# Kernel optimization log

Measured on AMD Instinct MI355X. Metric: run time of the kernel, lower is better.

The kernel has to match this reference:

```python
import jax, jax.numpy as jnp
import numpy as np

B, C, H, W = 4, 64, 64, 64
C8 = C // 8


def cl_attention(x, gamma):
    # DANet CAM-style channel attention: [B,C,H,W] -> [B,C,H,W]
    b, c, h, w = x.shape
    xf = x.reshape(b, c, h * w)                       # b c n
    energy = jnp.einsum('bcn,bdn->bcd', xf, xf)       # b c c
    energy = jnp.max(energy, axis=-1, keepdims=True) - energy
    attn = jax.nn.softmax(energy, axis=-1)
    out = jnp.einsum('bcd,bdn->bcn', attn, xf).reshape(b, c, h, w)
    return gamma * out + x


def setup_inputs() -> dict:
    key = jax.random.key(0)
    ks = jax.random.split(key, 8)
    s = 0.02
    return {
        'cnn_feat': jax.random.normal(ks[0], (B, C, H, W), jnp.float32),
        'vit_feat': jax.random.normal(ks[1], (B, C, H, W), jnp.float32),
        'Wq': jax.random.normal(ks[2], (C8, C), jnp.float32) * s,   # 1x1 conv kernel
        'bq': jnp.zeros((C8,), jnp.float32),
        'Wk': jax.random.normal(ks[3], (C8, C), jnp.float32) * s,
        'bk': jnp.zeros((C8,), jnp.float32),
        'Wv': jax.random.normal(ks[4], (C, C), jnp.float32) * s,
        'bv': jnp.zeros((C,), jnp.float32),
        'gamma': jnp.zeros((1,), jnp.float32),
        'gamma_cla_cnn': jnp.zeros((1,), jnp.float32),
        'gamma_cla_vit': jnp.zeros((1,), jnp.float32),
    }


def reference(cnn_feat, vit_feat, Wq, bq, Wk, bk, Wv, bv, gamma,
              gamma_cla_cnn, gamma_cla_vit):
    b, c, h, w = cnn_feat.shape
    n = h * w

    cnn_att = cl_attention(cnn_feat, gamma_cla_cnn)   # b c h w
    vit_att = cl_attention(vit_feat, gamma_cla_vit)   # b c h w

    # query: 1x1 conv -> view(b, C8, n) -> permute -> (b, n, C8)
    q = jnp.einsum('bchw,oc->bhwo', cnn_att, Wq).reshape(b, n, -1) + bq

    # vit: rearrange 'b c h w -> b (h w) c'
    vit_flat = vit_att.reshape(b, c, n).transpose(0, 2, 1)          # b n c
    k = vit_flat @ Wk.T + bk                                        # b n C8
    v = vit_flat @ Wv.T + bv                                        # b n C

    energy = jnp.einsum('bqd,bkd->bqk', q, k)                       # b n n
    attn = jax.nn.softmax(energy, axis=-1)
    out = jnp.einsum('bqk,bkc->bqc', attn, v)                       # b n c
    out = out.transpose(0, 2, 1).reshape(b, c, h, w)                # 'b (h w) c -> b c h w'
    return gamma * out + cnn_feat
```

## Files before the change

kernel.cpp:

```cpp
#include <hip/hip_runtime.h>
#include <hip/hip_bf16.h>

#define BSZ 4
#define CC 64
#define NN 4096
#define CN (CC*NN)
#define BCN (BSZ*CN)

typedef __attribute__((ext_vector_type(4))) float    f4v;
typedef __attribute__((ext_vector_type(4))) int      i4v;
typedef __attribute__((ext_vector_type(2))) int      i2v;
typedef __attribute__((ext_vector_type(2))) unsigned u2v;
typedef __attribute__((ext_vector_type(8))) short    s8v;

#define DPP_F(x_, ctrl_) __builtin_bit_cast(float, \
    __builtin_amdgcn_update_dpp(0, __builtin_bit_cast(int, (float)(x_)), (ctrl_), 0xf, 0xf, true))
#define QP_X1 0xB1

__device__ __forceinline__ unsigned pack_bf16(float lo, float hi) {
    unsigned l = __builtin_bit_cast(unsigned, lo);
    unsigned h = __builtin_bit_cast(unsigned, hi);
    return (h & 0xFFFF0000u) | (l >> 16);
}
__device__ __forceinline__ unsigned pack2(float lo, float hi) {
    float2 f2; f2.x = lo; f2.y = hi;
    __hip_bfloat162 h = __float22bfloat162_rn(f2);
    unsigned u;
    __builtin_memcpy(&u, &h, 4);
    return u;
}
__device__ __forceinline__ float blo(int d) {
    return __builtin_bit_cast(float, (unsigned)d << 16);
}
__device__ __forceinline__ float bhi(int d) {
    return __builtin_bit_cast(float, (unsigned)d & 0xFFFF0000u);
}

__global__ __launch_bounds__(256) void gram_k(const float* __restrict__ cnn,
                                              const float* __restrict__ vit,
                                              float* __restrict__ part) {
    __shared__ __align__(16) float sXT[128*68];
    int t = threadIdx.x;
    int blk = blockIdx.x;
    int ch = blk & 31, b = (blk >> 5) & 3, i2 = blk >> 7;
    const float* X = (i2 ? vit : cnn) + b * CN;
    int n0 = ch * 128;
#pragma unroll
    for (int j = 0; j < 8; j++) {
        int idx = t + j * 256;
        int c = idx >> 5, n4 = idx & 31;
        f4v val = *(const f4v*)&X[c * NN + n0 + n4 * 4];
        int base = (n4 * 4) * 68 + c;
        sXT[base]       = val[0];
        sXT[base + 68]  = val[1];
        sXT[base + 136] = val[2];
        sXT[base + 204] = val[3];
    }
    __syncthreads();
    int tc = (t & 15) * 4, td = (t >> 4) * 4;
    f4v acc[4];
#pragma unroll
    for (int i = 0; i < 4; i++) acc[i] = (f4v){0.f, 0.f, 0.f, 0.f};
    for (int k = 0; k < 128; k++) {
        f4v a  = *(const f4v*)&sXT[k * 68 + tc];
        f4v bb = *(const f4v*)&sXT[k * 68 + td];
#pragma unroll
        for (int i = 0; i < 4; i++) acc[i] += a[i] * bb;
    }
    float* dst = part + ch * 32768 + (i2 * 4 + b) * 4096;
#pragma unroll
    for (int i = 0; i < 4; i++) *(f4v*)&dst[(tc + i) * 64 + td] = acc[i];
}

__global__ void gred_k(const float* __restrict__ part, float* __restrict__ G) {
    int row = blockIdx.x;
    int d = threadIdx.x;
    float s = 0.f;
#pragma unroll 8
    for (int ch = 0; ch < 32; ch++) s += part[ch * 32768 + row * 64 + d];
    float mn = s;
#pragma unroll
    for (int off = 1; off < 64; off <<= 1) mn = fminf(mn, __shfl_xor(mn, off));
    float e = __expf(mn - s);
    float sm = e;
#pragma unroll
    for (int off = 1; off < 64; off <<= 1) sm += __shfl_xor(sm, off);
    G[row * 64 + d] = e / sm;
}

__global__ __launch_bounds__(256) void weff_k(const float* __restrict__ G,
                                              const float* __restrict__ Wq,
                                              const float* __restrict__ Wk,
                                              const float* __restrict__ Wv,
                                              const float* __restrict__ gcnn,
                                              const float* __restrict__ gvit,
                                              ushort* __restrict__ WeffB) {
    __shared__ float sA[8192];
    __shared__ float sWt[1024];
    int t = threadIdx.x;
    int b = blockIdx.x / 5, tile = blockIdx.x % 5;
    for (int i = t; i < 4096; i += 256) {
        sA[i]        = G[b * 4096 + i];
        sA[4096 + i] = G[(4 + b) * 4096 + i];
    }
    __syncthreads();
    float gc = *gcnn, gv = *gvit;
#pragma unroll
    for (int k = 0; k < 4; k++) {
        int idx = k * 256 + t;
        int r = idx >> 6, c = idx & 63;
        const float* Wrow; const float* A; float g;
        if (tile == 0) {
            if (r < 8) { Wrow = Wq + r * 64;       A = sA;        g = gc; }
            else       { Wrow = Wk + (r - 8) * 64; A = sA + 4096; g = gv; }
        } else         { Wrow = Wv + ((tile - 1) * 16 + r) * 64; A = sA + 4096; g = gv; }
        float s = 0.f;
#pragma unroll 8
        for (int d = 0; d < 64; d++) s += Wrow[d] * A[d * 64 + c];
        sWt[idx] = g * s + Wrow[c];
    }
    __syncthreads();
    if (t < 128) {
        int frag = t >> 6, lane = t & 63, m = lane & 15, q4 = lane >> 4;
        i4v o;
#pragma unroll
        for (int p = 0; p < 4; p++) {
            int c0 = frag * 32 + q4 * 8 + 2 * p;
            o[p] = (int)pack_bf16(sWt[m * 64 + c0], sWt[m * 64 + c0 + 1]);
        }
        *(i4v*)&WeffB[(size_t)(b * 10 + tile * 2 + frag) * 512 + lane * 8] = o;
    }
}

__global__ __launch_bounds__(256) void qkv_k(const float* __restrict__ cnn,
                                             const float* __restrict__ vit,
                                             const ushort* __restrict__ WeffB,
                                             const float* __restrict__ bq,
                                             const float* __restrict__ bk,
                                             const float* __restrict__ bv,
                                             ushort* __restrict__ qb, ushort* __restrict__ kb,
                                             ushort* __restrict__ vT) {
    int t = threadIdx.x;
    int b = blockIdx.x >> 6, n0 = (blockIdx.x & 63) * 64;
    int w = t >> 6, lane = t & 63, c15 = lane & 15, q4 = lane >> 4;
    int n = n0 + w * 16 + c15;
    const float LOG2E = 1.44269504f;

    s8v A[10];
    const ushort* WB = WeffB + (size_t)b * 5120 + lane * 8;
#pragma unroll
    for (int i = 0; i < 10; i++)
        A[i] = __builtin_bit_cast(s8v, *(const i4v*)(WB + (size_t)i * 512));

    s8v Bc[2], Bv[2];
#pragma unroll
    for (int f = 0; f < 2; f++) {
        i4v pc, pv;
#pragma unroll
        for (int p = 0; p < 4; p++) {
            int c0 = f * 32 + q4 * 8 + p * 2;
            size_t a0 = (size_t)b * CN + (size_t)c0 * NN + n;
            pc[p] = (int)pack_bf16(cnn[a0], cnn[a0 + NN]);
            pv[p] = (int)pack_bf16(vit[a0], vit[a0 + NN]);
        }
        Bc[f] = __builtin_bit_cast(s8v, pc);
        Bv[f] = __builtin_bit_cast(s8v, pv);
    }

    f4v acc = *(const f4v*)(bq + (q4 & 1) * 4);
    acc = __builtin_amdgcn_mfma_f32_16x16x32_bf16(A[0], Bc[0], acc, 0, 0, 0);
    acc = __builtin_amdgcn_mfma_f32_16x16x32_bf16(A[1], Bc[1], acc, 0, 0, 0);
    if (q4 < 2) {
        unsigned d0 = pack_bf16(acc[0] * LOG2E, acc[1] * LOG2E);
        unsigned d1 = pack_bf16(acc[2] * LOG2E, acc[3] * LOG2E);
        unsigned long long v = ((unsigned long long)d1 << 32) | d0;
        *(unsigned long long*)&qb[(size_t)(b * NN + n) * 8 + q4 * 4] = v;
    }
    acc = *(const f4v*)(bk + (q4 & 1) * 4);
    acc = __builtin_amdgcn_mfma_f32_16x16x32_bf16(A[0], Bv[0], acc, 0, 0, 0);
    acc = __builtin_amdgcn_mfma_f32_16x16x32_bf16(A[1], Bv[1], acc, 0, 0, 0);
    if (q4 >= 2) {
        unsigned d0 = pack_bf16(acc[0], acc[1]), d1 = pack_bf16(acc[2], acc[3]);
        unsigned long long v = ((unsigned long long)d1 << 32) | d0;
        *(unsigned long long*)&kb[(size_t)(b * NN + n) * 8 + (q4 - 2) * 4] = v;
    }
#pragma unroll
    for (int tile = 1; tile < 5; tile++) {
        acc = *(const f4v*)(bv + (tile - 1) * 16 + q4 * 4);
        acc = __builtin_amdgcn_mfma_f32_16x16x32_bf16(A[tile * 2],     Bv[0], acc, 0, 0, 0);
        acc = __builtin_amdgcn_mfma_f32_16x16x32_bf16(A[tile * 2 + 1], Bv[1], acc, 0, 0, 0);
#pragma unroll
        for (int r = 0; r < 4; r++) {
            float other = DPP_F(acc[r], QP_X1);
            unsigned pkd = (lane & 1) ? pack_bf16(other, acc[r])
                                      : pack_bf16(acc[r], other);
            if (!(lane & 1)) {
                int row = (tile - 1) * 16 + q4 * 4 + r;
                *(unsigned*)&vT[(size_t)(b * 64 + row) * NN + n] = pkd;
            }
        }
    }
}

__global__ __launch_bounds__(256, 2) void flash_k(const ushort* __restrict__ qb,
                                                  const ushort* __restrict__ kb,
                                                  const ushort* __restrict__ vT,
                                                  ushort* __restrict__ pOT,
                                                  float* __restrict__ pl) {
    __shared__ __align__(16) ushort Vlds[2 * 64 * 72];
    int t = threadIdx.x;
    int lane = t & 63, w = t >> 6;
    int c15 = lane & 15, q4 = lane >> 4;
    int blk = blockIdx.x;
    int s = blk >> 6, b = (blk >> 4) & 3, q0 = (blk & 15) * 256;

    s8v qB[4];
#pragma unroll
    for (int g = 0; g < 4; g++) {
        i4v qa = (i4v){0, 0, 0, 0};
        if (q4 == 0)
            qa = *(const i4v*)(qb + (size_t)(b * NN + q0 + w * 64 + g * 16 + c15) * 8);
        qB[g] = __builtin_bit_cast(s8v, qa);
    }

    f4v accO[4][4];
#pragma unroll
    for (int g = 0; g < 4; g++)
#pragma unroll
        for (int nt = 0; nt < 4; nt++) accO[g][nt] = (f4v){0.f, 0.f, 0.f, 0.f};
    float lacc[4] = {0.f, 0.f, 0.f, 0.f};

    const ushort* kbb = kb + (size_t)b * NN * 8 + (size_t)c15 * 8;

    int r = t >> 2, chk = t & 3;
    const ushort* vsrc = vT + (size_t)(b * 64 + r) * NN + chk * 16;
    int vdstoff = r * 72 + 32 * (chk >> 1) + 4 * (chk & 1);
    int vreadoff = c15 * 72 + 8 * q4;

    int kbase = s * 512;
    i4v bk_cur[4];
#pragma unroll
    for (int nt = 0; nt < 4; nt++)
        bk_cur[nt] = *(const i4v*)(kbb + (size_t)(kbase + nt * 16) * 8);
    i4v v0 = *(const i4v*)(vsrc + kbase);
    i4v v1 = *(const i4v*)(vsrc + kbase + 8);

    for (int kt = 0; kt < 8; kt++) {
        int k0 = kbase + kt * 64;
        ushort* vd = Vlds + (kt & 1) * 4608 + vdstoff;
        *(i2v*)(vd + 0)  = (i2v){v0[0], v0[1]};
        *(i2v*)(vd + 8)  = (i2v){v0[2], v0[3]};
        *(i2v*)(vd + 16) = (i2v){v1[0], v1[1]};
        *(i2v*)(vd + 24) = (i2v){v1[2], v1[3]};
        __syncthreads();

        const ushort* vb = Vlds + (kt & 1) * 4608 + vreadoff;
        i4v vA[2][4];
#pragma unroll
        for (int F = 0; F < 2; F++)
#pragma unroll
            for (int nt = 0; nt < 4; nt++)
                vA[F][nt] = *(const i4v*)(vb + nt * 16 * 72 + 32 * F);

        i4v bk_nxt[4];
        if (kt < 7) {
            v0 = *(const i4v*)(vsrc + k0 + 64);
            v1 = *(const i4v*)(vsrc + k0 + 64 + 8);
#pragma unroll
            for (int nt = 0; nt < 4; nt++)
                bk_nxt[nt] = *(const i4v*)(kbb + (size_t)(k0 + 64 + nt * 16) * 8);
        }

#pragma unroll
        for (int gp = 0; gp < 2; gp++) {
            f4v z = (f4v){0.f, 0.f, 0.f, 0.f};
            f4v S[2][4];
#pragma unroll
            for (int gg = 0; gg < 2; gg++)
#pragma unroll
                for (int nt = 0; nt < 4; nt++)
                    S[gg][nt] = __builtin_amdgcn_mfma_f32_16x16x32_bf16(
                        __builtin_bit_cast(s8v, bk_cur[nt]), qB[gp * 2 + gg],
                        z, 0, 0, 0);

            s8v Bp[2][2];
#pragma unroll
            for (int gg = 0; gg < 2; gg++) {
                f4v p[4];
                float ps = 0.f;
#pragma unroll
                for (int nt = 0; nt < 4; nt++)
#pragma unroll
                    for (int rr = 0; rr < 4; rr++) {
                        p[nt][rr] = __builtin_amdgcn_exp2f(S[gg][nt][rr]);
                        ps += p[nt][rr];
                    }
#pragma unroll
                for (int F = 0; F < 2; F++) {
                    i4v bp;
                    bp[0] = (int)pack2(p[2 * F][0],     p[2 * F][1]);
                    bp[1] = (int)pack2(p[2 * F][2],     p[2 * F][3]);
                    bp[2] = (int)pack2(p[2 * F + 1][0], p[2 * F + 1][1]);
                    bp[3] = (int)pack2(p[2 * F + 1][2], p[2 * F + 1][3]);
                    Bp[gg][F] = __builtin_bit_cast(s8v, bp);
                }
                lacc[gp * 2 + gg] += ps;
            }

#pragma unroll
            for (int F = 0; F < 2; F++)
#pragma unroll
                for (int gg = 0; gg < 2; gg++)
#pragma unroll
                    for (int nt = 0; nt < 4; nt++)
                        accO[gp * 2 + gg][nt] =
                            __builtin_amdgcn_mfma_f32_16x16x32_bf16(
                                __builtin_bit_cast(s8v, vA[F][nt]), Bp[gg][F],
                                accO[gp * 2 + gg][nt], 0, 0, 0);
        }
        if (kt < 7) {
#pragma unroll
            for (int nt = 0; nt < 4; nt++) bk_cur[nt] = bk_nxt[nt];
        }
    }

#pragma unroll
    for (int g = 0; g < 4; g++) {
        lacc[g] += __shfl_xor(lacc[g], 16);
        lacc[g] += __shfl_xor(lacc[g], 32);
    }

#pragma unroll
    for (int g = 0; g < 4; g++) {
        int qg = q0 + w * 64 + g * 16 + c15;
#pragma unroll
        for (int nt = 0; nt < 4; nt++) {
            int cg = nt * 4 + q4;
            u2v d;
            d[0] = pack2(accO[g][nt][0], accO[g][nt][1]);
            d[1] = pack2(accO[g][nt][2], accO[g][nt][3]);
            *(u2v*)&pOT[((size_t)((s * 4 + b) * 16 + cg) * NN + qg) * 4] = d;
        }
        if (q4 == 0)
            pl[(size_t)(s * 4 + b) * NN + qg] = lacc[g];
    }
}

__global__ __launch_bounds__(256) void comb_k(const ushort* __restrict__ pOT,
                                              const float* __restrict__ pl,
                                              const float* __restrict__ cnn,
                                              const float* __restrict__ gamma,
                                              float* __restrict__ out) {
    int t = threadIdx.x;
    int b = blockIdx.x >> 6, n0 = (blockIdx.x & 63) * 64;
    int nq = t & 15, cl = t >> 4;
    int n = n0 + nq * 4;
    f4v L = (f4v){0.f, 0.f, 0.f, 0.f};
#pragma unroll
    for (int s = 0; s < 8; s++)
        L += *(const f4v*)&pl[(size_t)(s * 4 + b) * NN + n];
    float g = *gamma;
    f4v rv;
#pragma unroll
    for (int j = 0; j < 4; j++) rv[j] = g / L[j];

    f4v Oc[4];
#pragma unroll
    for (int cc = 0; cc < 4; cc++) Oc[cc] = (f4v){0.f, 0.f, 0.f, 0.f};
#pragma unroll
    for (int s = 0; s < 8; s++) {
        const ushort* src = pOT + ((size_t)((s * 4 + b) * 16 + cl) * NN + n) * 4;
        i4v a  = *(const i4v*)src;
        i4v bb = *(const i4v*)(src + 8);
        Oc[0][0] += blo(a[0]);  Oc[1][0] += bhi(a[0]);
        Oc[2][0] += blo(a[1]);  Oc[3][0] += bhi(a[1]);
        Oc[0][1] += blo(a[2]);  Oc[1][1] += bhi(a[2]);
        Oc[2][1] += blo(a[3]);  Oc[3][1] += bhi(a[3]);
        Oc[0][2] += blo(bb[0]); Oc[1][2] += bhi(bb[0]);
        Oc[2][2] += blo(bb[1]); Oc[3][2] += bhi(bb[1]);
        Oc[0][3] += blo(bb[2]); Oc[1][3] += bhi(bb[2]);
        Oc[2][3] += blo(bb[3]); Oc[3][3] += bhi(bb[3]);
    }
#pragma unroll
    for (int cc = 0; cc < 4; cc++) {
        size_t gi = (size_t)(b * 64 + cl * 4 + cc) * NN + n;
        f4v cv = *(const f4v*)&cnn[gi];
        *(f4v*)&out[gi] = Oc[cc] * rv + cv;
    }
}

extern "C" void kernel_launch(void* const* d_in, const int* in_sizes, int n_in,
                              void* d_out, int out_size, void* d_ws, size_t ws_size,
                              hipStream_t stream) {
    const float* cnn  = (const float*)d_in[0];
    const float* vit  = (const float*)d_in[1];
    const float* Wq   = (const float*)d_in[2];
    const float* bq   = (const float*)d_in[3];
    const float* Wk   = (const float*)d_in[4];
    const float* bk   = (const float*)d_in[5];
    const float* Wv   = (const float*)d_in[6];
    const float* bv   = (const float*)d_in[7];
    const float* gam  = (const float*)d_in[8];
    const float* gcnn = (const float*)d_in[9];
    const float* gvit = (const float*)d_in[10];
    float* out = (float*)d_out;

    float* ws = (float*)d_ws;
    ushort* pOT   = (ushort*)ws;
    float*  part  = ws;
    float*  G     = ws + 8388608;
    ushort* WeffB = (ushort*)(ws + 8421376);
    ushort* qb    = (ushort*)(ws + 8431616);
    ushort* kb    = (ushort*)(ws + 8497152);
    ushort* vT    = (ushort*)(ws + 8562688);
    float*  pl    = ws + 9086976;

    gram_k <<<256, 256, 0, stream>>>(cnn, vit, part);
    gred_k <<<512, 64,  0, stream>>>(part, G);
    weff_k <<<20,  256, 0, stream>>>(G, Wq, Wk, Wv, gcnn, gvit, WeffB);
    qkv_k  <<<256, 256, 0, stream>>>(cnn, vit, WeffB, bq, bk, bv, qb, kb, vT);
    flash_k<<<512, 256, 0, stream>>>(qb, kb, vT, pOT, pl);
    comb_k <<<256, 256, 0, stream>>>(pOT, pl, cnn, gam, out);
}
```

Before: 129.7 us.

## Rebalance flash split-K: fewer key splits, smaller query tiles, prioritize MFMA

The flash kernel now uses 128 queries per block (32 per wave) and 4 key splits of 1024 keys each, instead of 256 queries per block and 8 splits of 512. This halves the partial outputs that comb_k must read and reduce, and lowers per-wave register pressure. It also adds s_setprio around the PV MFMA block and unroll pragmas on the flash and gram loops. In exchange, each loaded K/V tile is reused by fewer queries, so global and LDS traffic per useful FLOP goes up. The grid size is unchanged at 512 blocks.

```diff
diff --git a/kernel.cpp b/kernel.cpp
--- a/kernel.cpp
+++ b/kernel.cpp
@@ -61,6 +61,7 @@
     f4v acc[4];
 #pragma unroll
     for (int i = 0; i < 4; i++) acc[i] = (f4v){0.f, 0.f, 0.f, 0.f};
+#pragma unroll 4
     for (int k = 0; k < 128; k++) {
         f4v a  = *(const f4v*)&sXT[k * 68 + tc];
         f4v bb = *(const f4v*)&sXT[k * 68 + td];
@@ -212,23 +213,23 @@
     int lane = t & 63, w = t >> 6;
     int c15 = lane & 15, q4 = lane >> 4;
     int blk = blockIdx.x;
-    int s = blk >> 6, b = (blk >> 4) & 3, q0 = (blk & 15) * 256;
-
-    s8v qB[4];
-#pragma unroll
-    for (int g = 0; g < 4; g++) {
+    int s = blk >> 7, b = (blk >> 5) & 3, q0 = (blk & 31) * 128;
+
+    s8v qB[2];
+#pragma unroll
+    for (int g = 0; g < 2; g++) {
         i4v qa = (i4v){0, 0, 0, 0};
         if (q4 == 0)
-            qa = *(const i4v*)(qb + (size_t)(b * NN + q0 + w * 64 + g * 16 + c15) * 8);
+            qa = *(const i4v*)(qb + (size_t)(b * NN + q0 + w * 32 + g * 16 + c15) * 8);
         qB[g] = __builtin_bit_cast(s8v, qa);
     }
 
-    f4v accO[4][4];
-#pragma unroll
-    for (int g = 0; g < 4; g++)
+    f4v accO[2][4];
+#pragma unroll
+    for (int g = 0; g < 2; g++)
 #pragma unroll
         for (int nt = 0; nt < 4; nt++) accO[g][nt] = (f4v){0.f, 0.f, 0.f, 0.f};
-    float lacc[4] = {0.f, 0.f, 0.f, 0.f};
+    float lacc[2] = {0.f, 0.f};
 
     const ushort* kbb = kb + (size_t)b * NN * 8 + (size_t)c15 * 8;
 
@@ -237,7 +238,7 @@
     int vdstoff = r * 72 + 32 * (chk >> 1) + 4 * (chk & 1);
     int vreadoff = c15 * 72 + 8 * q4;
 
-    int kbase = s * 512;
+    int kbase = s * 1024;
     i4v bk_cur[4];
 #pragma unroll
     for (int nt = 0; nt < 4; nt++)
@@ -245,7 +246,8 @@
     i4v v0 = *(const i4v*)(vsrc + kbase);
     i4v v1 = *(const i4v*)(vsrc + kbase + 8);
 
-    for (int kt = 0; kt < 8; kt++) {
+#pragma unroll 2
+    for (int kt = 0; kt < 16; kt++) {
         int k0 = kbase + kt * 64;
         ushort* vd = Vlds + (kt & 1) * 4608 + vdstoff;
         *(i2v*)(vd + 0)  = (i2v){v0[0], v0[1]};
@@ -263,7 +265,7 @@
                 vA[F][nt] = *(const i4v*)(vb + nt * 16 * 72 + 32 * F);
 
         i4v bk_nxt[4];
-        if (kt < 7) {
+        if (kt < 15) {
             v0 = *(const i4v*)(vsrc + k0 + 64);
             v1 = *(const i4v*)(vsrc + k0 + 64 + 8);
 #pragma unroll
@@ -271,68 +273,67 @@
                 bk_nxt[nt] = *(const i4v*)(kbb + (size_t)(k0 + 64 + nt * 16) * 8);
         }
 
-#pragma unroll
-        for (int gp = 0; gp < 2; gp++) {
-            f4v z = (f4v){0.f, 0.f, 0.f, 0.f};
-            f4v S[2][4];
-#pragma unroll
-            for (int gg = 0; gg < 2; gg++)
+        f4v z = (f4v){0.f, 0.f, 0.f, 0.f};
+        f4v S[2][4];
+#pragma unroll
+        for (int g = 0; g < 2; g++)
+#pragma unroll
+            for (int nt = 0; nt < 4; nt++)
+                S[g][nt] = __builtin_amdgcn_mfma_f32_16x16x32_bf16(
+                    __builtin_bit_cast(s8v, bk_cur[nt]), qB[g], z, 0, 0, 0);
+
+        s8v Bp[2][2];
+#pragma unroll
+        for (int g = 0; g < 2; g++) {
+            f4v p[4];
+            float ps = 0.f;
+#pragma unroll
+            for (int nt = 0; nt < 4; nt++)
+#pragma unroll
+                for (int rr = 0; rr < 4; rr++) {
+                    p[nt][rr] = __builtin_amdgcn_exp2f(S[g][nt][rr]);
+                    ps += p[nt][rr];
+                }
+#pragma unroll
+            for (int F = 0; F < 2; F++) {
+                i4v bp;
+                bp[0] = (int)pack2(p[2 * F][0],     p[2 * F][1]);
+                bp[1] = (int)pack2(p[2 * F][2],     p[2 * F][3]);
+                bp[2] = (int)pack2(p[2 * F + 1][0], p[2 * F + 1][1]);
+                bp[3] = (int)pack2(p[2 * F + 1][2], p[2 * F + 1][3]);
+                Bp[g][F] = __builtin_bit_cast(s8v, bp);
+            }
+            lacc[g] += ps;
+        }
+
+        __builtin_amdgcn_s_setprio(1);
+#pragma unroll
+        for (int F = 0; F < 2; F++)
+#pragma unroll
+            for (int g = 0; g < 2; g++)
 #pragma unroll
                 for (int nt = 0; nt < 4; nt++)
-                    S[gg][nt] = __builtin_amdgcn_mfma_f32_16x16x32_bf16(
-                        __builtin_bit_cast(s8v, bk_cur[nt]), qB[gp * 2 + gg],
-                        z, 0, 0, 0);
-
-            s8v Bp[2][2];
-#pragma unroll
-            for (int gg = 0; gg < 2; gg++) {
-                f4v p[4];
-                float ps = 0.f;
-#pragma unroll
-                for (int nt = 0; nt < 4; nt++)
-#pragma unroll
-                    for (int rr = 0; rr < 4; rr++) {
-                        p[nt][rr] = __builtin_amdgcn_exp2f(S[gg][nt][rr]);
-                        ps += p[nt][rr];
-                    }
-#pragma unroll
-                for (int F = 0; F < 2; F++) {
-                    i4v bp;
-                    bp[0] = (int)pack2(p[2 * F][0],     p[2 * F][1]);
-                    bp[1] = (int)pack2(p[2 * F][2],     p[2 * F][3]);
-                    bp[2] = (int)pack2(p[2 * F + 1][0], p[2 * F + 1][1]);
-                    bp[3] = (int)pack2(p[2 * F + 1][2], p[2 * F + 1][3]);
-                    Bp[gg][F] = __builtin_bit_cast(s8v, bp);
-                }
-                lacc[gp * 2 + gg] += ps;
-            }
-
-#pragma unroll
-            for (int F = 0; F < 2; F++)
-#pragma unroll
-                for (int gg = 0; gg < 2; gg++)
-#pragma unroll
-                    for (int nt = 0; nt < 4; nt++)
-                        accO[gp * 2 + gg][nt] =
-                            __builtin_amdgcn_mfma_f32_16x16x32_bf16(
-                                __builtin_bit_cast(s8v, vA[F][nt]), Bp[gg][F],
-                                accO[gp * 2 + gg][nt], 0, 0, 0);
-        }
-        if (kt < 7) {
+                    accO[g][nt] =
+                        __builtin_amdgcn_mfma_f32_16x16x32_bf16(
+                            __builtin_bit_cast(s8v, vA[F][nt]), Bp[g][F],
+                            accO[g][nt], 0, 0, 0);
+        __builtin_amdgcn_s_setprio(0);
+
+        if (kt < 15) {
 #pragma unroll
             for (int nt = 0; nt < 4; nt++) bk_cur[nt] = bk_nxt[nt];
         }
     }
 
 #pragma unroll
-    for (int g = 0; g < 4; g++) {
+    for (int g = 0; g < 2; g++) {
         lacc[g] += __shfl_xor(lacc[g], 16);
         lacc[g] += __shfl_xor(lacc[g], 32);
     }
 
 #pragma unroll
-    for (int g = 0; g < 4; g++) {
-        int qg = q0 + w * 64 + g * 16 + c15;
+    for (int g = 0; g < 2; g++) {
+        int qg = q0 + w * 32 + g * 16 + c15;
 #pragma unroll
         for (int nt = 0; nt < 4; nt++) {
             int cg = nt * 4 + q4;
@@ -357,7 +358,7 @@
     int n = n0 + nq * 4;
     f4v L = (f4v){0.f, 0.f, 0.f, 0.f};
 #pragma unroll
-    for (int s = 0; s < 8; s++)
+    for (int s = 0; s < 4; s++)
         L += *(const f4v*)&pl[(size_t)(s * 4 + b) * NN + n];
     float g = *gamma;
     f4v rv;
@@ -368,7 +369,7 @@
 #pragma unroll
     for (int cc = 0; cc < 4; cc++) Oc[cc] = (f4v){0.f, 0.f, 0.f, 0.f};
 #pragma unroll
-    for (int s = 0; s < 8; s++) {
+    for (int s = 0; s < 4; s++) {
         const ushort* src = pOT + ((size_t)((s * 4 + b) * 16 + cl) * NN + n) * 4;
         i4v a  = *(const i4v*)src;
         i4v bb = *(const i4v*)(src + 8);
```

After: 126.6 us. 1.02x faster.
